# Optimization experiments

Hardware: AMD Instinct MI355X
Metric: run time of the kernel (lower is better)

## Reference

```python
import jax, jax.numpy as jnp
import numpy as np

# model dims
B_, S_, D_ = 2, 2048, 1024
D_STATE, EXPAND, HEADDIM, CHUNK, NGROUPS = 128, 2, 64, 64, 1
D_INNER = EXPAND * D_
NHEADS = D_INNER // HEADDIM  # 32 ssd heads
D_PROJ = 2 * D_INNER + 2 * NGROUPS * D_STATE + NHEADS  # 4384
H_, KV_, HD_ = 16, 4, 64  # attention heads / kv heads / head dim
ROPE_DIMS = 16
MLP_DIM = int(3.0 * D_)


def _rmsnorm(x, w=None, eps=1e-5):
    y = x * jax.lax.rsqrt(jnp.mean(x * x, axis=-1, keepdims=True) + eps)
    return y * w if w is not None else y


def _layernorm(x, w, b, eps=1e-5):
    m = jnp.mean(x, axis=-1, keepdims=True)
    v = jnp.mean((x - m) ** 2, axis=-1, keepdims=True)
    return (x - m) * jax.lax.rsqrt(v + eps) * w + b


def _segsum(x):
    # (..., T) -> (..., T, T) lower-tri cumulative sums, -inf above diag
    T = x.shape[-1]
    i = jnp.arange(T)
    xx = jnp.where(i[:, None] > i[None, :], jnp.broadcast_to(x[..., None], x.shape + (T,)), 0.0)
    s = jnp.cumsum(xx, axis=-2)
    return jnp.where(i[:, None] >= i[None, :], s, -jnp.inf)


def _ssd_chunked(x, A, B, C, chunk):
    # x:(b,s,h,p) A:(b,s,h) B,C:(b,s,g,n)
    b, s, h, p = x.shape
    g, n = B.shape[2], B.shape[3]
    if g < h:
        B = jnp.repeat(B, h // g, axis=2)
        C = jnp.repeat(C, h // g, axis=2)
    c = s // chunk
    x = x.reshape(b, c, chunk, h, p)
    A = A.reshape(b, c, chunk, h).transpose(0, 3, 1, 2)  # b h c l
    B = B.reshape(b, c, chunk, h, n)
    C = C.reshape(b, c, chunk, h, n)
    L = jnp.exp(_segsum(A))
    Y_diag = jnp.einsum('bclhn,bcshn,bhcls,bcshp->bclhp', C, B, L, x)
    A_cum = jnp.cumsum(A, axis=-1)
    decay_states = jnp.exp(A_cum[..., -1:] - A_cum)
    states = jnp.einsum('bclhn,bhcl,bclhp->bchpn', B, decay_states, x)
    decay_chunk = jnp.exp(_segsum(jnp.pad(A_cum[..., -1], ((0, 0), (0, 0), (1, 0)))))
    new_states = jnp.einsum('bhzc,bchpn->bzhpn', decay_chunk[:, :, :c, 1:c + 1], states)
    Y_off = jnp.einsum('bclhn,bchpn,bhcl->bclhp', C, new_states, jnp.exp(A_cum))
    return (Y_diag + Y_off).reshape(b, s, h, p)


def _rope_cos_sin(s, rd, base=10000.0):
    inv = 1.0 / base ** (jnp.arange(0, rd, 2, dtype=jnp.float32) / rd)
    f = jnp.outer(jnp.arange(s, dtype=jnp.float32), inv)  # (s, rd/2)
    return jnp.cos(f)[None, :, None, :], jnp.sin(f)[None, :, None, :]


def _apply_rope(x, cos, sin, rd):
    xr, xp = x[..., :rd], x[..., rd:]
    half = rd // 2
    x1, x2 = xr[..., :half], xr[..., half:]
    xr = jnp.concatenate([x1 * cos + x2 * sin, -x1 * sin + x2 * cos], axis=-1)
    return jnp.concatenate([xr, xp], axis=-1)


def _mamba_block(x, mnorm_w, in_w, out_w, Dp, dt_b, A_log, Bn_w, Cn_w):
    b, s, _ = x.shape
    h = _rmsnorm(x, mnorm_w)
    zxbcdt = h @ in_w.T
    z, xs, Bc, Cc, dt = jnp.split(
        zxbcdt,
        [D_INNER, 2 * D_INNER, 2 * D_INNER + NGROUPS * D_STATE, 2 * D_INNER + 2 * NGROUPS * D_STATE],
        axis=-1)
    dt = jax.nn.softplus(dt + dt_b)  # (b,s,nheads)
    A = -jnp.exp(A_log)  # (nheads,)
    xs = xs.reshape(b, s, NHEADS, HEADDIM)
    Bc = _rmsnorm(Bc.reshape(b, s, NGROUPS, D_STATE), Bn_w)
    Cc = _rmsnorm(Cc.reshape(b, s, NGROUPS, D_STATE), Cn_w)
    y = _ssd_chunked(xs * dt[..., None], A[None, None, :] * dt, Bc, Cc, CHUNK)
    y = y + xs * Dp[None, None, :, None]
    y = y * jax.nn.silu(z).reshape(b, s, NHEADS, HEADDIM)
    return x + y.reshape(b, s, D_INNER) @ out_w.T


def _attn_block(x, ln1_w, ln1_b, cq_w, ck_w, cv_w, cproj_w, q_gain, ln2_w, ln2_b, fc_w, proj_w):
    b, s, d = x.shape
    h = _layernorm(x, ln1_w, ln1_b)
    q = (h @ cq_w.T).reshape(b, s, H_, HD_)
    k = (h @ ck_w.T).reshape(b, s, KV_, HD_)
    v = (h @ cv_w.T).reshape(b, s, KV_, HD_)
    eps = jnp.finfo(x.dtype).eps
    q = _rmsnorm(q, eps=eps)
    k = _rmsnorm(k, eps=eps)
    cos, sin = _rope_cos_sin(s, ROPE_DIMS)
    q = _apply_rope(q, cos, sin, ROPE_DIMS)
    k = _apply_rope(k, cos, sin, ROPE_DIMS)
    q = q * q_gain[None, None, :, None]
    rep = H_ // KV_
    k = jnp.repeat(k, rep, axis=2)
    v = jnp.repeat(v, rep, axis=2)
    scores = jnp.einsum('bqhd,bkhd->bhqk', q, k) / np.float32(np.sqrt(HD_))
    i = jnp.arange(s)
    scores = jnp.where(i[:, None] >= i[None, :], scores, -jnp.inf)
    w = jax.nn.softmax(scores, axis=-1)
    y = jnp.einsum('bhqk,bkhd->bqhd', w, v).reshape(b, s, d)
    x = x + y @ cproj_w.T
    h = _layernorm(x, ln2_w, ln2_b)
    return x + jax.nn.silu(h @ fc_w.T) @ proj_w.T


def setup_inputs() -> dict:
    key = jax.random.key(0)
    ks = jax.random.split(key, 16)
    rn = lambda k, shp, sc=0.02: (jax.random.normal(k, shp, dtype=jnp.float32) * sc)
    return {
        'x': jax.random.normal(ks[0], (B_, S_, D_), dtype=jnp.float32),
        'mnorm_w': jnp.ones((D_,), jnp.float32),
        'in_proj_w': rn(ks[1], (D_PROJ, D_)),
        'out_proj_w': rn(ks[2], (D_, D_INNER)),
        'D_param': jnp.ones((NHEADS,), jnp.float32),
        'dt_bias': rn(ks[3], (NHEADS,), 0.1),
        'A_log': jnp.log(0.5 + jax.random.uniform(ks[4], (NHEADS,), dtype=jnp.float32) * 0.5),
        'Bn_w': jnp.ones((D_STATE,), jnp.float32),
        'Cn_w': jnp.ones((D_STATE,), jnp.float32),
        'ln1_w': jnp.ones((D_,), jnp.float32),
        'ln1_b': jnp.zeros((D_,), jnp.float32),
        'cq_w': rn(ks[5], (D_, D_)),
        'ck_w': rn(ks[6], (KV_ * HD_, D_)),
        'cv_w': rn(ks[7], (KV_ * HD_, D_)),
        'cproj_w': rn(ks[8], (D_, D_)),
        'q_gain': jnp.full((H_,), 5.25, jnp.float32),
        'ln2_w': jnp.ones((D_,), jnp.float32),
        'ln2_b': jnp.zeros((D_,), jnp.float32),
        'fc_w': rn(ks[9], (MLP_DIM, D_)),
        'proj_w': rn(ks[10], (D_, MLP_DIM)),
    }


def reference(x, mnorm_w, in_proj_w, out_proj_w, D_param, dt_bias, A_log, Bn_w, Cn_w,
              ln1_w, ln1_b, cq_w, ck_w, cv_w, cproj_w, q_gain, ln2_w, ln2_b, fc_w, proj_w):
    x = _mamba_block(x, mnorm_w, in_proj_w, out_proj_w, D_param, dt_bias, A_log, Bn_w, Cn_w)
    x = _attn_block(x, ln1_w, ln1_b, cq_w, ck_w, cv_w, cproj_w, q_gain, ln2_w, ln2_b, fc_w, proj_w)
    return x
```

## Files before the change

### kernel.cpp

```cpp
#include <hip/hip_runtime.h>
#include <hip/hip_bf16.h>
#include <math.h>

#define B_    2
#define S_    2048
#define D_    1024
#define DI    2048
#define NH    32
#define HD    64
#define DS    128
#define CH    64
#define NC    32
#define DP    4384
#define HATT  16
#define KVH   4
#define RD    16
#define MLP   3072
#define ROWS  (B_*S_)

typedef __bf16 bf16;
typedef __bf16 bf16x8 __attribute__((ext_vector_type(8)));
typedef __bf16 bf16x4 __attribute__((ext_vector_type(4)));
typedef float  f32x4  __attribute__((ext_vector_type(4)));

__device__ __forceinline__ void async_copy16(const void* g, void* l) {
  __builtin_amdgcn_global_load_lds(
      (const __attribute__((address_space(1))) unsigned int*)g,
      (__attribute__((address_space(3))) unsigned int*)l, 16, 0, 0);
}

__device__ __forceinline__ float waveReduceSum(float v) {
#pragma unroll
  for (int off = 32; off > 0; off >>= 1) v += __shfl_down(v, off, 64);
  return v;
}

template<int NW>
__device__ __forceinline__ float blockReduceSum(float v, float* sh) {
  v = waveReduceSum(v);
  int lane = threadIdx.x & 63, wid = threadIdx.x >> 6;
  if (lane == 0) sh[wid] = v;
  __syncthreads();
  float s = 0.f;
#pragma unroll
  for (int i = 0; i < NW; i++) s += sh[i];
  __syncthreads();
  return s;
}

struct CastSeg { const float* src; bf16* dst; int nval; int ntot; int blk0; };
struct CastArgs { CastSeg seg[8]; };

__global__ __launch_bounds__(256) void castw_all(CastArgs a) {
  int blk = blockIdx.x;
  int si = 0;
#pragma unroll
  for (int i = 1; i < 8; i++) if (blk >= a.seg[i].blk0) si = i;
  CastSeg s = a.seg[si];
  int i = ((blk - s.blk0) * 256 + threadIdx.x) * 4;
  if (i >= s.ntot) return;
  float4 v = {0.f, 0.f, 0.f, 0.f};
  if (i < s.nval) v = *(const float4*)(s.src + i);
  bf16x4 o;
  o[0] = (bf16)v.x; o[1] = (bf16)v.y; o[2] = (bf16)v.z; o[3] = (bf16)v.w;
  *(bf16x4*)(s.dst + i) = o;
}

__global__ __launch_bounds__(256) void rmsnorm_k(const float* __restrict__ x,
                                                 const float* __restrict__ w,
                                                 bf16* __restrict__ y, int n) {
  __shared__ float sh[4];
  size_t row = blockIdx.x;
  const float* xr = x + row * n;
  bf16* yr = y + row * n;
  float ss = 0.f;
  for (int i = threadIdx.x; i < n; i += 256) { float v = xr[i]; ss += v * v; }
  ss = blockReduceSum<4>(ss, sh);
  float inv = rsqrtf(ss / n + 1e-5f);
  for (int i = threadIdx.x; i < n; i += 256) yr[i] = (bf16)(xr[i] * inv * w[i]);
}

template<int ACT, typename OT>
__global__ __launch_bounds__(256) void gemm_mfma(const bf16* __restrict__ A,
                                                 const bf16* __restrict__ W,
                                                 const float* __restrict__ R,
                                                 OT* __restrict__ C,
                                                 int M, int N, int K) {
  __shared__ bf16 As[128 * 32];
  __shared__ bf16 Ws[128 * 32];
  int tid = threadIdx.x, lane = tid & 63, wave = tid >> 6;
  int mt = M >> 7;
  int bid = blockIdx.x;
  int bm = (bid % mt) * 128, bn = (bid / mt) * 128;
  const bf16* gA0 = A + (size_t)(bm + wave * 32 + (lane >> 2)) * K + (lane & 3) * 8;
  const bf16* gA1 = gA0 + (size_t)16 * K;
  const bf16* gW0 = W + (size_t)(bn + wave * 32 + (lane >> 2)) * K + (lane & 3) * 8;
  const bf16* gW1 = gW0 + (size_t)16 * K;
  bf16* lA0 = As + wave * 32 * 32;
  bf16* lA1 = lA0 + 16 * 32;
  bf16* lW0 = Ws + wave * 32 * 32;
  bf16* lW1 = lW0 + 16 * 32;
  int fr = lane & 15, fq = lane >> 4;
  int wm = wave >> 1, wn = wave & 1;
  const bf16* pA = As + (wm * 64 + fr) * 32 + fq * 8;
  const bf16* pW = Ws + (wn * 64 + fr) * 32 + fq * 8;
  f32x4 acc[4][4] = {};
  for (int k0 = 0; k0 < K; k0 += 32) {
    async_copy16(gA0, lA0);
    async_copy16(gA1, lA1);
    async_copy16(gW0, lW0);
    async_copy16(gW1, lW1);
    gA0 += 32; gA1 += 32; gW0 += 32; gW1 += 32;
    __syncthreads();
    bf16x8 af[4], bfr[4];
#pragma unroll
    for (int mi = 0; mi < 4; mi++) af[mi] = *(const bf16x8*)(pA + mi * 16 * 32);
#pragma unroll
    for (int ni = 0; ni < 4; ni++) bfr[ni] = *(const bf16x8*)(pW + ni * 16 * 32);
#pragma unroll
    for (int mi = 0; mi < 4; mi++)
#pragma unroll
      for (int ni = 0; ni < 4; ni++)
        acc[mi][ni] = __builtin_amdgcn_mfma_f32_16x16x32_bf16(af[mi], bfr[ni], acc[mi][ni], 0, 0, 0);
    __syncthreads();
  }
#pragma unroll
  for (int mi = 0; mi < 4; mi++) {
    int row = bm + wm * 64 + mi * 16 + fq * 4;
#pragma unroll
    for (int ni = 0; ni < 4; ni++) {
      int col = bn + wn * 64 + ni * 16 + fr;
      if (col < N) {
#pragma unroll
        for (int r = 0; r < 4; r++) {
          float v = acc[mi][ni][r];
          if (ACT == 1) v = v / (1.f + __expf(-v));
          if (R) v += R[(size_t)(row + r) * N + col];
          C[(size_t)(row + r) * N + col] = (OT)v;
        }
      }
    }
  }
}

__global__ __launch_bounds__(256) void gemm_sk(const bf16* __restrict__ A,
                                               const bf16* __restrict__ W,
                                               bf16* __restrict__ P,
                                               int M, int N, int K, int kchunk) {
  __shared__ bf16 As[128 * 32];
  __shared__ bf16 Ws[128 * 32];
  int tid = threadIdx.x, lane = tid & 63, wave = tid >> 6;
  int mt = M >> 7;
  int bid = blockIdx.x;
  int bm = (bid % mt) * 128, bn = (bid / mt) * 128;
  int ks = blockIdx.z;
  int kbeg = ks * kchunk;
  const bf16* gA0 = A + (size_t)(bm + wave * 32 + (lane >> 2)) * K + kbeg + (lane & 3) * 8;
  const bf16* gA1 = gA0 + (size_t)16 * K;
  const bf16* gW0 = W + (size_t)(bn + wave * 32 + (lane >> 2)) * K + kbeg + (lane & 3) * 8;
  const bf16* gW1 = gW0 + (size_t)16 * K;
  bf16* lA0 = As + wave * 32 * 32;
  bf16* lA1 = lA0 + 16 * 32;
  bf16* lW0 = Ws + wave * 32 * 32;
  bf16* lW1 = lW0 + 16 * 32;
  int fr = lane & 15, fq = lane >> 4;
  int wm = wave >> 1, wn = wave & 1;
  const bf16* pA = As + (wm * 64 + fr) * 32 + fq * 8;
  const bf16* pW = Ws + (wn * 64 + fr) * 32 + fq * 8;
  f32x4 acc[4][4] = {};
  for (int k0 = 0; k0 < kchunk; k0 += 32) {
    async_copy16(gA0, lA0);
    async_copy16(gA1, lA1);
    async_copy16(gW0, lW0);
    async_copy16(gW1, lW1);
    gA0 += 32; gA1 += 32; gW0 += 32; gW1 += 32;
    __syncthreads();
    bf16x8 af[4], bfr[4];
#pragma unroll
    for (int mi = 0; mi < 4; mi++) af[mi] = *(const bf16x8*)(pA + mi * 16 * 32);
#pragma unroll
    for (int ni = 0; ni < 4; ni++) bfr[ni] = *(const bf16x8*)(pW + ni * 16 * 32);
#pragma unroll
    for (int mi = 0; mi < 4; mi++)
#pragma unroll
      for (int ni = 0; ni < 4; ni++)
        acc[mi][ni] = __builtin_amdgcn_mfma_f32_16x16x32_bf16(af[mi], bfr[ni], acc[mi][ni], 0, 0, 0);
    __syncthreads();
  }
  bf16* Pp = P + (size_t)ks * M * N;
#pragma unroll
  for (int mi = 0; mi < 4; mi++) {
    int row = bm + wm * 64 + mi * 16 + fq * 4;
#pragma unroll
    for (int ni = 0; ni < 4; ni++) {
      int col = bn + wn * 64 + ni * 16 + fr;
#pragma unroll
      for (int r = 0; r < 4; r++)
        Pp[(size_t)(row + r) * N + col] = (bf16)acc[mi][ni][r];
    }
  }
}

__global__ __launch_bounds__(256) void reduce_ln2(const bf16* __restrict__ p0,
                                                  const bf16* __restrict__ p1,
                                                  const float* __restrict__ res,
                                                  const float* __restrict__ w,
                                                  const float* __restrict__ b,
                                                  float* __restrict__ xo,
                                                  bf16* __restrict__ ho) {
  __shared__ float sh[4];
  size_t o = (size_t)blockIdx.x * 1024;
  int i = threadIdx.x * 4;
  bf16x4 a = *(const bf16x4*)(p0 + o + i);
  bf16x4 c = *(const bf16x4*)(p1 + o + i);
  f32x4 rv = *(const f32x4*)(res + o + i);
  f32x4 v;
  float s = 0.f, s2 = 0.f;
#pragma unroll
  for (int j = 0; j < 4; j++) {
    v[j] = (float)a[j] + (float)c[j] + rv[j];
    s += v[j]; s2 += v[j] * v[j];
  }
  s  = blockReduceSum<4>(s,  sh);
  s2 = blockReduceSum<4>(s2, sh);
  float mean = s / 1024.f;
  float var  = s2 / 1024.f - mean * mean;
  float inv  = rsqrtf(var + 1e-5f);
  f32x4 wv = *(const f32x4*)(w + i);
  f32x4 bv = *(const f32x4*)(b + i);
  *(f32x4*)(xo + o + i) = v;
  bf16x4 hv;
#pragma unroll
  for (int j = 0; j < 4; j++) hv[j] = (bf16)((v[j] - mean) * inv * wv[j] + bv[j]);
  *(bf16x4*)(ho + o + i) = hv;
}

__global__ __launch_bounds__(256) void reduce_out3(const bf16* __restrict__ p0,
                                                   const bf16* __restrict__ p1,
                                                   const bf16* __restrict__ p2,
                                                   const float* __restrict__ res,
                                                   float* __restrict__ out) {
  int i = (blockIdx.x * 256 + threadIdx.x) * 4;
  bf16x4 a = *(const bf16x4*)(p0 + i);
  bf16x4 c = *(const bf16x4*)(p1 + i);
  bf16x4 d = *(const bf16x4*)(p2 + i);
  f32x4 v = *(const f32x4*)(res + i);
#pragma unroll
  for (int j = 0; j < 4; j++) v[j] += (float)a[j] + (float)c[j] + (float)d[j];
  *(f32x4*)(out + i) = v;
}

__global__ __launch_bounds__(256) void reduce_qkv(const bf16* __restrict__ P,
                                                  const float* __restrict__ q_gain,
                                                  bf16* __restrict__ q,
                                                  bf16* __restrict__ k,
                                                  bf16* __restrict__ v) {
  __shared__ float buf[1536];
  size_t row = blockIdx.x;
  size_t o = row * 1536;
  const bf16* p0 = P + o;
  const bf16* p1 = P + (size_t)ROWS * 1536 + o;
  int tid = threadIdx.x;
  for (int i = tid; i < 384; i += 256) {
    bf16x4 a = *(const bf16x4*)(p0 + i * 4);
    bf16x4 c = *(const bf16x4*)(p1 + i * 4);
    f32x4 vv;
#pragma unroll
    for (int j = 0; j < 4; j++) vv[j] = (float)a[j] + (float)c[j];
    *(f32x4*)(buf + i * 4) = vv;
  }
  __syncthreads();
  int lane = tid & 63, w = tid >> 6;
  int s = (int)(row & (S_ - 1));
  int ri = lane & 7;
  float rinv = __expf(-(float)ri * (0.125f * 9.210340371976184f));
  float ang = (float)s * rinv;
  float cs = cosf(ang), sn = sinf(ang);
#pragma unroll
  for (int j = 0; j < 6; j++) {
    int hh = w * 6 + j;
    float val = buf[hh * 64 + lane];
    if (hh < 20) {
      float ss = val * val;
#pragma unroll
      for (int off = 32; off > 0; off >>= 1) ss += __shfl_xor(ss, off, 64);
      val *= rsqrtf(ss / 64.f + 1.1920929e-7f);
      float other = __shfl_xor(val, 8, 64);
      float res = val;
      if (lane < RD) res = (lane < 8) ? (val * cs + other * sn) : (val * cs - other * sn);
      if (hh < 16) {
        res *= q_gain[hh];
        q[row * (HATT * HD) + hh * HD + lane] = (bf16)res;
      } else {
        k[row * (KVH * HD) + (hh - 16) * HD + lane] = (bf16)res;
      }
    } else {
      v[row * (KVH * HD) + (hh - 20) * HD + lane] = (bf16)val;
    }
  }
}

__global__ __launch_bounds__(256) void gemm_inproj(const bf16* __restrict__ A,
                                                   const bf16* __restrict__ W,
                                                   bf16* __restrict__ zt,
                                                   bf16* __restrict__ xt,
                                                   bf16* __restrict__ bcdt) {
  const int K = 1024;
  __shared__ bf16 As[128 * 32];
  __shared__ bf16 Ws[128 * 32];
  __shared__ bf16 Ts[64 * 136];
  int tid = threadIdx.x, lane = tid & 63, wave = tid >> 6;
  int bid = blockIdx.x;
  int bm = (bid & 31) * 128, bn = (bid >> 5) * 128;
  const bf16* gA0 = A + (size_t)(bm + wave * 32 + (lane >> 2)) * K + (lane & 3) * 8;
  const bf16* gA1 = gA0 + (size_t)16 * K;
  const bf16* gW0 = W + (size_t)(bn + wave * 32 + (lane >> 2)) * K + (lane & 3) * 8;
  const bf16* gW1 = gW0 + (size_t)16 * K;
  bf16* lA0 = As + wave * 32 * 32;
  bf16* lA1 = lA0 + 16 * 32;
  bf16* lW0 = Ws + wave * 32 * 32;
  bf16* lW1 = lW0 + 16 * 32;
  int fr = lane & 15, fq = lane >> 4;
  int wm = wave >> 1, wn = wave & 1;
  const bf16* pA = As + (wm * 64 + fr) * 32 + fq * 8;
  const bf16* pW = Ws + (wn * 64 + fr) * 32 + fq * 8;
  f32x4 acc[4][4] = {};
  for (int k0 = 0; k0 < K; k0 += 32) {
    async_copy16(gA0, lA0);
    async_copy16(gA1, lA1);
    async_copy16(gW0, lW0);
    async_copy16(gW1, lW1);
    gA0 += 32; gA1 += 32; gW0 += 32; gW1 += 32;
    __syncthreads();
    bf16x8 af[4], bfr[4];
#pragma unroll
    for (int mi = 0; mi < 4; mi++) af[mi] = *(const bf16x8*)(pA + mi * 16 * 32);
#pragma unroll
    for (int ni = 0; ni < 4; ni++) bfr[ni] = *(const bf16x8*)(pW + ni * 16 * 32);
#pragma unroll
    for (int mi = 0; mi < 4; mi++)
#pragma unroll
      for (int ni = 0; ni < 4; ni++)
        acc[mi][ni] = __builtin_amdgcn_mfma_f32_16x16x32_bf16(af[mi], bfr[ni], acc[mi][ni], 0, 0, 0);
    __syncthreads();
  }
  if (bn < 4096) {
    bf16* base = (bn < 2048) ? zt : xt;
    int bq = bm >> 11, bmS = bm & 2047;
#pragma unroll
    for (int p = 0; p < 2; p++) {
      __syncthreads();
      if (wn == p) {
#pragma unroll
        for (int mi = 0; mi < 4; mi++)
#pragma unroll
          for (int ni = 0; ni < 4; ni++) {
            bf16x4 o;
#pragma unroll
            for (int r = 0; r < 4; r++) o[r] = (bf16)acc[mi][ni][r];
            *(bf16x4*)(Ts + (ni * 16 + fr) * 136 + wm * 64 + mi * 16 + fq * 4) = o;
          }
      }
      __syncthreads();
      int hh = ((bn & 2047) + p * 64) >> 6;
      bf16* dst = base + ((size_t)(bq * NH + hh) * HD) * S_ + bmS;
#pragma unroll
      for (int i = 0; i < 4; i++) {
        int idx = tid + i * 256;
        int cl = idx >> 4, sgc = (idx & 15) * 8;
        *(bf16x8*)(dst + (size_t)cl * S_ + sgc) = *(const bf16x8*)(Ts + cl * 136 + sgc);
      }
    }
  } else {
#pragma unroll
    for (int mi = 0; mi < 4; mi++) {
      int row0m = bm + wm * 64 + mi * 16 + fq * 4;
#pragma unroll
      for (int ni = 0; ni < 4; ni++) {
        int col = bn + wn * 64 + ni * 16 + fr;
        if (col < 4384) {
#pragma unroll
          for (int r = 0; r < 4; r++)
            bcdt[(size_t)(row0m + r) * 288 + (col - 4096)] = (bf16)acc[mi][ni][r];
        }
      }
    }
  }
}

__global__ __launch_bounds__(256) void t64(const bf16* __restrict__ in, bf16* __restrict__ out,
                                           int istr, size_t io, size_t oo, int n_nt) {
  __shared__ bf16 T[64 * 72];
  int bid = blockIdx.x;
  int st = bid & 31;
  int nt = (bid >> 5) % n_nt;
  int outer = bid / (32 * n_nt);
  const bf16* ip = in + outer * io + (size_t)st * 64 * istr + nt * 64;
  int tid = threadIdx.x;
#pragma unroll
  for (int i = 0; i < 2; i++) {
    int cid = tid + i * 256; int s = cid >> 3, pc = (cid & 7) * 8;
    *(bf16x8*)(T + s * 72 + pc) = *(const bf16x8*)(ip + (size_t)s * istr + pc);
  }
  __syncthreads();
  bf16* op = out + outer * oo + (size_t)nt * 64 * 2048 + st * 64;
#pragma unroll
  for (int i = 0; i < 2; i++) {
    int cid = tid + i * 256; int p = cid >> 3, sc = (cid & 7) * 8;
    bf16x8 o;
#pragma unroll
    for (int j = 0; j < 8; j++) o[j] = T[(sc + j) * 72 + p];
    *(bf16x8*)(op + (size_t)p * 2048 + sc) = o;
  }
}

__global__ __launch_bounds__(64) void ssd_prep(const bf16* __restrict__ bcdt,
                                               const float* __restrict__ dt_bias,
                                               const float* __restrict__ A_log,
                                               float* __restrict__ dt_c,
                                               float* __restrict__ ddc,
                                               float* __restrict__ ac_c,
                                               float* __restrict__ T_out) {
  int bid = blockIdx.x;
  int c = bid % NC, hh = (bid / NC) % NH, b = bid / (NC * NH);
  int l = threadIdx.x;
  size_t row = (size_t)b * S_ + c * 64 + l;
  float raw = (float)bcdt[row * 288 + 256 + hh] + dt_bias[hh];
  float dtv = (raw > 20.f) ? raw : log1pf(__expf(raw));
  float a = -__expf(A_log[hh]) * dtv;
  float ps = a;
#pragma unroll
  for (int off = 1; off < 64; off <<= 1) {
    float t = __shfl_up(ps, off, 64);
    if (l >= off) ps += t;
  }
  float a63 = __shfl(ps, 63, 64);
  size_t o = ((size_t)b * NH + hh) * S_ + c * 64 + l;
  dt_c[o] = dtv;
  ac_c[o] = ps;
  ddc[o] = __expf(a63 - ps) * dtv;
  if (l == 63) T_out[(b * NH + hh) * NC + c] = ps;
}

__global__ __launch_bounds__(128) void bc_norm(const bf16* __restrict__ bcdt,
                                               const float* __restrict__ Bw,
                                               const float* __restrict__ Cw,
                                               bf16* __restrict__ Bn,
                                               bf16* __restrict__ Cn) {
  __shared__ float shb[2], shc[2];
  size_t row = blockIdx.x;
  int i = threadIdx.x;
  float bv = (float)bcdt[row * 288 + i];
  float cv = (float)bcdt[row * 288 + 128 + i];
  float sb = waveReduceSum(bv * bv);
  float sc = waveReduceSum(cv * cv);
  int lane = threadIdx.x & 63, wid = threadIdx.x >> 6;
  if (lane == 0) { shb[wid] = sb; shc[wid] = sc; }
  __syncthreads();
  float tb = shb[0] + shb[1];
  float tc = shc[0] + shc[1];
  Bn[row * DS + i] = (bf16)(bv * rsqrtf(tb / DS + 1e-5f) * Bw[i]);
  Cn[row * DS + i] = (bf16)(cv * rsqrtf(tc / DS + 1e-5f) * Cw[i]);
}

__global__ __launch_bounds__(256) void ssd_states(const bf16* __restrict__ Xt,
                                                  const bf16* __restrict__ Btr,
                                                  const float* __restrict__ ddc,
                                                  bf16* __restrict__ states) {
  __shared__ bf16 Xs[64 * 72];
  __shared__ bf16 Bs[128 * 72];
  int bid = blockIdx.x;
  int h = bid % NH;
  int c = (bid / NH) % NC;
  int b = bid / (NH * NC);
  int tid = threadIdx.x, lane = tid & 63, w = tid >> 6;
  int fr = lane & 15, fq = lane >> 4;
  const size_t xbase = (size_t)(b * NH + h) * HD * S_ + c * 64;
  const size_t dbase = (size_t)(b * NH + h) * S_ + c * 64;
#pragma unroll
  for (int i = 0; i < 2; i++) {
    int cid = tid + i * 256; int p = cid >> 3, sc = (cid & 7) * 8;
    bf16x8 xv = *(const bf16x8*)(Xt + xbase + (size_t)p * S_ + sc);
    f32x4 d0 = *(const f32x4*)(ddc + dbase + sc);
    f32x4 d1 = *(const f32x4*)(ddc + dbase + sc + 4);
    bf16x8 o;
#pragma unroll
    for (int j = 0; j < 4; j++) { o[j] = (bf16)((float)xv[j] * d0[j]); o[4 + j] = (bf16)((float)xv[4 + j] * d1[j]); }
    *(bf16x8*)(Xs + p * 72 + sc) = o;
  }
  const size_t bbase = (size_t)b * 128 * S_ + c * 64;
#pragma unroll
  for (int i = 0; i < 4; i++) {
    int cid = tid + i * 256; int n = cid >> 3, sc = (cid & 7) * 8;
    *(bf16x8*)(Bs + n * 72 + sc) = *(const bf16x8*)(Btr + bbase + (size_t)n * S_ + sc);
  }
  __syncthreads();
  f32x4 acc[4][2] = {};
#pragma unroll
  for (int ks = 0; ks < 2; ks++) {
    bf16x8 a[4], bb[2];
#pragma unroll
    for (int pt = 0; pt < 4; pt++) a[pt] = *(const bf16x8*)(Xs + (pt * 16 + fr) * 72 + ks * 32 + fq * 8);
#pragma unroll
    for (int n2 = 0; n2 < 2; n2++) bb[n2] = *(const bf16x8*)(Bs + ((2 * w + n2) * 16 + fr) * 72 + ks * 32 + fq * 8);
#pragma unroll
    for (int pt = 0; pt < 4; pt++)
#pragma unroll
      for (int n2 = 0; n2 < 2; n2++)
        acc[pt][n2] = __builtin_amdgcn_mfma_f32_16x16x32_bf16(a[pt], bb[n2], acc[pt][n2], 0, 0, 0);
  }
  bf16* outp = states + (size_t)bid * 8192;
#pragma unroll
  for (int pt = 0; pt < 4; pt++)
#pragma unroll
    for (int n2 = 0; n2 < 2; n2++) {
      int n = (2 * w + n2) * 16 + fr;
#pragma unroll
      for (int r = 0; r < 4; r++)
        outp[(size_t)(pt * 16 + fq * 4 + r) * 128 + n] = (bf16)acc[pt][n2][r];
    }
}

__global__ __launch_bounds__(256) void ssd_scan(bf16* __restrict__ states,
                                                const float* __restrict__ T) {
  __shared__ float eT[NC];
  int part = blockIdx.x & 7;
  int bh = blockIdx.x >> 3;
  int b = bh / NH, h = bh % NH;
  if (threadIdx.x < NC) eT[threadIdx.x] = __expf(T[(size_t)(b * NH + h) * NC + threadIdx.x]);
  __syncthreads();
  const size_t cstride = (size_t)NH * HD * DS;
  size_t base = ((size_t)b * NC * NH + h) * (HD * DS);
#pragma unroll
  for (int j = 0; j < 4; j++) {
    int e = part * 1024 + threadIdx.x + j * 256;
    float carry = 0.f;
    size_t idx = base + e;
    for (int c = 0; c < NC; c++) {
      float sv = (float)states[idx];
      states[idx] = (bf16)carry;
      carry = sv + eT[c] * carry;
      idx += cstride;
    }
  }
}

__global__ __launch_bounds__(256) void ssd_out(const bf16* __restrict__ Cn,
                                               const bf16* __restrict__ Bn,
                                               const bf16* __restrict__ Xt,
                                               const bf16* __restrict__ Zt,
                                               const float* __restrict__ dt_c,
                                               const float* __restrict__ ac_c,
                                               const bf16* __restrict__ states,
                                               const float* __restrict__ Dp,
                                               bf16* __restrict__ ybf) {
  __shared__ bf16 Cs[64 * 136];
  __shared__ bf16 BNs[64 * 136];
  __shared__ bf16 Xs[64 * 72];
  __shared__ bf16 G[64 * 72];
  __shared__ float acs[64];
  int bid = blockIdx.x;
  int h = bid % NH;
  int c = (bid / NH) % NC;
  int b = bid / (NH * NC);
  int tid = threadIdx.x, lane = tid & 63, w = tid >> 6;
  int fr = lane & 15, fq = lane >> 4;
  size_t row0 = (size_t)b * S_ + c * 64;
  const size_t abase = (size_t)(b * NH + h) * S_ + c * 64;
  if (tid < 64) acs[tid] = ac_c[abase + tid];
#pragma unroll
  for (int i = 0; i < 4; i++) {
    int cid = tid + i * 256; int l = cid >> 4, nc = (cid & 15) * 8;
    float e = __expf(ac_c[abase + l]);
    bf16x8 cv = *(const bf16x8*)(Cn + (row0 + l) * DS + nc);
    bf16x8 o;
#pragma unroll
    for (int j = 0; j < 8; j++) o[j] = (bf16)((float)cv[j] * e);
    *(bf16x8*)(Cs + l * 136 + nc) = o;
    *(bf16x8*)(BNs + l * 136 + nc) = *(const bf16x8*)(Bn + (row0 + l) * DS + nc);
  }
  const size_t xbase = (size_t)(b * NH + h) * HD * S_ + c * 64;
#pragma unroll
  for (int i = 0; i < 2; i++) {
    int cid = tid + i * 256; int p = cid >> 3, sc = (cid & 7) * 8;
    bf16x8 xv = *(const bf16x8*)(Xt + xbase + (size_t)p * S_ + sc);
    f32x4 d0 = *(const f32x4*)(dt_c + abase + sc);
    f32x4 d1 = *(const f32x4*)(dt_c + abase + sc + 4);
    bf16x8 o;
#pragma unroll
    for (int j = 0; j < 4; j++) { o[j] = (bf16)((float)xv[j] * d0[j]); o[4 + j] = (bf16)((float)xv[4 + j] * d1[j]); }
    *(bf16x8*)(Xs + p * 72 + sc) = o;
  }
  __syncthreads();
  bf16x8 ca[4];
#pragma unroll
  for (int ks = 0; ks < 4; ks++) ca[ks] = *(const bf16x8*)(Cs + (w * 16 + fr) * 136 + ks * 32 + fq * 8);
  f32x4 cb[4] = {};
  for (int st = 0; st <= w; st++)
#pragma unroll
    for (int ks = 0; ks < 4; ks++)
      cb[st] = __builtin_amdgcn_mfma_f32_16x16x32_bf16(ca[ks],
                 *(const bf16x8*)(BNs + (st * 16 + fr) * 136 + ks * 32 + fq * 8), cb[st], 0, 0, 0);
#pragma unroll
  for (int st = 0; st < 4; st++) {
    float es = (st <= w) ? __expf(-acs[st * 16 + fr]) : 0.f;
#pragma unroll
    for (int r = 0; r < 4; r++) {
      int lloc = fq * 4 + r;
      float g = 0.f;
      if (st < w) g = cb[st][r] * es;
      else if (st == w) g = (lloc >= fr) ? cb[st][r] * es : 0.f;
      G[(w * 16 + lloc) * 72 + st * 16 + fr] = (bf16)g;
    }
  }
  f32x4 acc[4] = {};
  {
    bf16x8 ga0 = *(const bf16x8*)(G + (w * 16 + fr) * 72 + fq * 8);
    bf16x8 ga1 = *(const bf16x8*)(G + (w * 16 + fr) * 72 + 32 + fq * 8);
#pragma unroll
    for (int pt = 0; pt < 4; pt++) {
      acc[pt] = __builtin_amdgcn_mfma_f32_16x16x32_bf16(ga0,
                  *(const bf16x8*)(Xs + (pt * 16 + fr) * 72 + fq * 8), acc[pt], 0, 0, 0);
      acc[pt] = __builtin_amdgcn_mfma_f32_16x16x32_bf16(ga1,
                  *(const bf16x8*)(Xs + (pt * 16 + fr) * 72 + 32 + fq * 8), acc[pt], 0, 0, 0);
    }
  }
  __syncthreads();
  const bf16* stp = states + (size_t)bid * 8192;
#pragma unroll
  for (int i = 0; i < 4; i++) {
    int cid = tid + i * 256; int p = cid >> 4, nc = (cid & 15) * 8;
    *(bf16x8*)(BNs + p * 136 + nc) = *(const bf16x8*)(stp + (size_t)p * 128 + nc);
  }
  __syncthreads();
#pragma unroll
  for (int pt = 0; pt < 4; pt++)
#pragma unroll
    for (int ks = 0; ks < 4; ks++)
      acc[pt] = __builtin_amdgcn_mfma_f32_16x16x32_bf16(ca[ks],
                  *(const bf16x8*)(BNs + (pt * 16 + fr) * 136 + ks * 32 + fq * 8), acc[pt], 0, 0, 0);
  float dph = Dp[h];
#pragma unroll
  for (int pt = 0; pt < 4; pt++) {
    int p = pt * 16 + fr;
    size_t tb = (xbase + (size_t)p * S_) + w * 16 + fq * 4;
    bf16x4 xs4 = *(const bf16x4*)(Xt + tb);
    bf16x4 z4  = *(const bf16x4*)(Zt + tb);
#pragma unroll
    for (int r = 0; r < 4; r++) {
      int l = w * 16 + fq * 4 + r;
      float yv = acc[pt][r] + (float)xs4[r] * dph;
      float z = (float)z4[r];
      yv *= z / (1.f + __expf(-z));
      ybf[((row0 + l) * NH + h) * HD + p] = (bf16)yv;
    }
  }
}

#define KSTR 72
#define PSTR 72
__global__ __launch_bounds__(256) void attn_mfma(const bf16* __restrict__ q,
                                                 const bf16* __restrict__ k,
                                                 const bf16* __restrict__ vtr,
                                                 bf16* __restrict__ Po,
                                                 float* __restrict__ Ls) {
  __shared__ bf16 Ks[64 * KSTR];
  __shared__ bf16 Vs[64 * KSTR];
  __shared__ bf16 Pl[4][32 * PSTR];
  int c = 39 - blockIdx.x;
  int g = (c < 4) ? 0 : (c < 12) ? 1 : (c < 24) ? 2 : 3;
  int gbase = (g == 0) ? 0 : (g == 1) ? 4 : (g == 2) ? 12 : 24;
  int d = c - gbase;
  int qt = 4 * g + d / (g + 1);
  int sk = d % (g + 1);
  int h = blockIdx.y, b = blockIdx.z;
  int kvh = h >> 2;
  int tid = threadIdx.x, lane = tid & 63, w = tid >> 6;
  int fr = lane & 15, fq = lane >> 4;
  const float SC = 0.18033688011112042f;
  const float M2 = 62.0f;
  int kt0 = sk * 8;
  int ktend = min(kt0 + 8, 2 * qt + 2);
  int qbase = qt * 128 + w * 32;
  int qmaxw = qbase + 31;
  bf16x8 bq[2][2];
#pragma unroll
  for (int qc = 0; qc < 2; qc++)
#pragma unroll
    for (int ks = 0; ks < 2; ks++)
      bq[qc][ks] = *(const bf16x8*)(q + (size_t)(b * S_ + qbase + qc * 16 + fr) * (HATT * HD)
                                      + h * HD + ks * 32 + fq * 8);
  int sr = tid >> 3, sc8 = (tid & 7) * 8;
  const bf16* kg = k + ((size_t)(b * S_) + sr) * (KVH * HD) + kvh * HD + sc8;
  const bf16* vg = vtr + ((size_t)(b * KVH + kvh) * HD + sr) * S_ + sc8;
  bf16x8 krg0, krg1, vrg0, vrg1;
  {
    const bf16* kp = kg + (size_t)kt0 * 64 * (KVH * HD);
    const bf16* vp = vg + (size_t)kt0 * 64;
    krg0 = *(const bf16x8*)(kp);
    krg1 = *(const bf16x8*)(kp + (size_t)32 * (KVH * HD));
    vrg0 = *(const bf16x8*)(vp);
    vrg1 = *(const bf16x8*)(vp + (size_t)32 * S_);
  }
  float lsum[2] = {0.f, 0.f};
  f32x4 yacc[2][4] = {};
  bf16* Plw = Pl[w];
  for (int kt = kt0; kt < ktend; kt++) {
    __syncthreads();
    *(bf16x8*)(&Ks[sr * KSTR + sc8]) = krg0;
    *(bf16x8*)(&Ks[(sr + 32) * KSTR + sc8]) = krg1;
    *(bf16x8*)(&Vs[sr * KSTR + sc8]) = vrg0;
    *(bf16x8*)(&Vs[(sr + 32) * KSTR + sc8]) = vrg1;
    __syncthreads();
    if ((kt + 1) < ktend) {
      const bf16* kp = kg + (size_t)(kt + 1) * 64 * (KVH * HD);
      const bf16* vp = vg + (size_t)(kt + 1) * 64;
      krg0 = *(const bf16x8*)(kp);
      krg1 = *(const bf16x8*)(kp + (size_t)32 * (KVH * HD));
      vrg0 = *(const bf16x8*)(vp);
      vrg1 = *(const bf16x8*)(vp + (size_t)32 * S_);
    }
    if (kt * 64 <= qmaxw) {
      bool nomask = (kt * 64 + 63) <= qbase;
      if (nomask) {
#pragma unroll
        for (int mi = 0; mi < 4; mi++) {
          const bf16* krow = &Ks[(mi * 16 + fr) * KSTR];
          bf16x8 ak0 = *(const bf16x8*)(krow + fq * 8);
          bf16x8 ak1 = *(const bf16x8*)(krow + 32 + fq * 8);
#pragma unroll
          for (int qc = 0; qc < 2; qc++) {
            f32x4 s = {};
            s = __builtin_amdgcn_mfma_f32_16x16x32_bf16(ak0, bq[qc][0], s, 0, 0, 0);
            s = __builtin_amdgcn_mfma_f32_16x16x32_bf16(ak1, bq[qc][1], s, 0, 0, 0);
            bf16x4 pk;
#pragma unroll
            for (int r = 0; r < 4; r++) {
              float p = __builtin_amdgcn_exp2f(s[r] * SC - M2);
              lsum[qc] += p;
              pk[r] = (bf16)p;
            }
            *(bf16x4*)(Plw + (qc * 16 + fr) * PSTR + mi * 16 + fq * 4) = pk;
          }
        }
      } else {
#pragma unroll
        for (int mi = 0; mi < 4; mi++) {
          int s0 = kt * 64 + mi * 16;
          if (s0 > qmaxw) {
            bf16x4 zz = {};
#pragma unroll
            for (int qc = 0; qc < 2; qc++)
              *(bf16x4*)(Plw + (qc * 16 + fr) * PSTR + mi * 16 + fq * 4) = zz;
          } else {
            const bf16* krow = &Ks[(mi * 16 + fr) * KSTR];
            bf16x8 ak0 = *(const bf16x8*)(krow + fq * 8);
            bf16x8 ak1 = *(const bf16x8*)(krow + 32 + fq * 8);
#pragma unroll
            for (int qc = 0; qc < 2; qc++) {
              f32x4 s = {};
              s = __builtin_amdgcn_mfma_f32_16x16x32_bf16(ak0, bq[qc][0], s, 0, 0, 0);
              s = __builtin_amdgcn_mfma_f32_16x16x32_bf16(ak1, bq[qc][1], s, 0, 0, 0);
              int qq = qbase + qc * 16 + fr;
              bf16x4 pk;
#pragma unroll
              for (int r = 0; r < 4; r++) {
                int sp = s0 + fq * 4 + r;
                float p = (sp <= qq) ? __builtin_amdgcn_exp2f(s[r] * SC - M2) : 0.f;
                lsum[qc] += p;
                pk[r] = (bf16)p;
              }
              *(bf16x4*)(Plw + (qc * 16 + fr) * PSTR + mi * 16 + fq * 4) = pk;
            }
          }
        }
      }
#pragma unroll
      for (int ks2 = 0; ks2 < 2; ks2++) {
        bf16x8 bp[2];
#pragma unroll
        for (int qc = 0; qc < 2; qc++)
          bp[qc] = *(const bf16x8*)(Plw + (qc * 16 + fr) * PSTR + ks2 * 32 + fq * 8);
#pragma unroll
        for (int pi = 0; pi < 4; pi++) {
          bf16x8 av = *(const bf16x8*)(&Vs[(pi * 16 + fr) * KSTR + ks2 * 32 + fq * 8]);
#pragma unroll
          for (int qc = 0; qc < 2; qc++)
            yacc[qc][pi] = __builtin_amdgcn_mfma_f32_16x16x32_bf16(av, bp[qc], yacc[qc][pi], 0, 0, 0);
        }
      }
    }
  }
#pragma unroll
  for (int qc = 0; qc < 2; qc++) {
    lsum[qc] += __shfl_xor(lsum[qc], 16, 64);
    lsum[qc] += __shfl_xor(lsum[qc], 32, 64);
    int qrow = qt * 128 + w * 32 + qc * 16 + fr;
    if (fq == 0)
      Ls[((size_t)(b * 16 + h) * 2048 + qrow) * 4 + sk] = lsum[qc];
    bf16* pop = Po + ((((size_t)(b * 16 + h) * 16 + qt) * 4 + sk) * 128
                       + w * 32 + qc * 16 + fr) * 64 + fq * 4;
#pragma unroll
    for (int pi = 0; pi < 4; pi++) {
      bf16x4 o;
#pragma unroll
      for (int r = 0; r < 4; r++) o[r] = (bf16)yacc[qc][pi][r];
      *(bf16x4*)(pop + pi * 16) = o;
    }
  }
}

__global__ __launch_bounds__(256) void attn_red(const bf16* __restrict__ Po,
                                                const float* __restrict__ Ls,
                                                bf16* __restrict__ y2) {
  int row = blockIdx.x;
  int b = row >> 11;
  int qrow = row & 2047;
  int qt = qrow >> 7, r = qrow & 127;
  int nch = (qt >> 2) + 1;
  int t = threadIdx.x;
  int h = t >> 4, e4 = (t & 15) << 2;
  const float* lp = Ls + ((size_t)(b * 16 + h) * 2048 + qrow) * 4;
  float ls = 0.f;
  f32x4 acc = {};
  for (int sk = 0; sk < nch; sk++) {
    ls += lp[sk];
    const bf16* pp = Po + ((((size_t)(b * 16 + h) * 16 + qt) * 4 + sk) * 128 + r) * 64 + e4;
    bf16x4 v = *(const bf16x4*)(pp);
#pragma unroll
    for (int j = 0; j < 4; j++) acc[j] += (float)v[j];
  }
  float inv = 1.f / ls;
  bf16x4 o;
#pragma unroll
  for (int j = 0; j < 4; j++) o[j] = (bf16)(acc[j] * inv);
  *(bf16x4*)(y2 + (size_t)row * 1024 + h * 64 + e4) = o;
}

constexpr size_t OFF_WIN  = 0;
constexpr size_t OFF_WOUT = 9175040;
constexpr size_t OFF_WQKV = 13369344;
constexpr size_t OFF_WCP  = 16515072;
constexpr size_t OFF_WFC  = 18612224;
constexpr size_t OFF_WPR  = 24903680;
constexpr size_t OFF_HBF  = 31195136;
constexpr size_t OFF_BCDT = 39583744;
constexpr size_t OFF_XT   = 41943040;
constexpr size_t OFF_ZT   = 58720256;
constexpr size_t OFF_DTC  = 75497472;
constexpr size_t OFF_DDC  = 76546048;
constexpr size_t OFF_ACC  = 77594624;
constexpr size_t OFF_T    = 78643200;
constexpr size_t OFF_BN   = 78651392;
constexpr size_t OFF_CN   = 79699968;
constexpr size_t OFF_BTR  = 80748544;
constexpr size_t OFF_ST   = 81797120;
constexpr size_t OFF_YBF  = 148905984;
constexpr size_t OFF_X1   = 165683200;
constexpr size_t OFF_P    = OFF_ST;
constexpr size_t OFF_PO   = OFF_ST;
constexpr size_t OFF_LS   = OFF_BCDT;
constexpr size_t OFF_QB   = OFF_XT;
constexpr size_t OFF_KB   = OFF_XT + 8388608;
constexpr size_t OFF_VB   = OFF_XT + 10485760;
constexpr size_t OFF_VTR  = OFF_XT + 12582912;
constexpr size_t OFF_Y2   = OFF_ZT;
constexpr size_t OFF_X2   = 50331648;
constexpr size_t OFF_MLP  = 132128768;

extern "C" void kernel_launch(void* const* d_in, const int* in_sizes, int n_in,
                              void* d_out, int out_size, void* d_ws, size_t ws_size,
                              hipStream_t stream) {
  (void)in_sizes; (void)n_in; (void)out_size; (void)ws_size;
  const float* x        = (const float*)d_in[0];
  const float* mnorm_w  = (const float*)d_in[1];
  const float* in_w     = (const float*)d_in[2];
  const float* out_w    = (const float*)d_in[3];
  const float* Dp       = (const float*)d_in[4];
  const float* dt_bias  = (const float*)d_in[5];
  const float* A_log    = (const float*)d_in[6];
  const float* Bn_w     = (const float*)d_in[7];
  const float* Cn_w     = (const float*)d_in[8];
  const float* ln1_w    = (const float*)d_in[9];
  const float* ln1_b    = (const float*)d_in[10];
  const float* cq_w     = (const float*)d_in[11];
  const float* ck_w     = (const float*)d_in[12];
  const float* cv_w     = (const float*)d_in[13];
  const float* cproj_w  = (const float*)d_in[14];
  const float* q_gain   = (const float*)d_in[15];
  const float* ln2_w    = (const float*)d_in[16];
  const float* ln2_b    = (const float*)d_in[17];
  const float* fc_w     = (const float*)d_in[18];
  const float* proj_w   = (const float*)d_in[19];
  float* out = (float*)d_out;
  char* W8 = (char*)d_ws;

  bf16* w_in   = (bf16*)(W8 + OFF_WIN);
  bf16* w_out  = (bf16*)(W8 + OFF_WOUT);
  bf16* w_qkv  = (bf16*)(W8 + OFF_WQKV);
  bf16* w_cp   = (bf16*)(W8 + OFF_WCP);
  bf16* w_fc   = (bf16*)(W8 + OFF_WFC);
  bf16* w_pr   = (bf16*)(W8 + OFF_WPR);
  bf16* h_bf   = (bf16*)(W8 + OFF_HBF);
  bf16* bcdt   = (bf16*)(W8 + OFF_BCDT);
  bf16* Xt     = (bf16*)(W8 + OFF_XT);
  bf16* Zt     = (bf16*)(W8 + OFF_ZT);
  float* dt_c  = (float*)(W8 + OFF_DTC);
  float* ddc   = (float*)(W8 + OFF_DDC);
  float* ac_c  = (float*)(W8 + OFF_ACC);
  float* Tb    = (float*)(W8 + OFF_T);
  bf16* Bn     = (bf16*)(W8 + OFF_BN);
  bf16* Cn     = (bf16*)(W8 + OFF_CN);
  bf16* Btr    = (bf16*)(W8 + OFF_BTR);
  bf16* st     = (bf16*)(W8 + OFF_ST);
  bf16* ybf    = (bf16*)(W8 + OFF_YBF);
  float* x1    = (float*)(W8 + OFF_X1);
  bf16* Pbuf   = (bf16*)(W8 + OFF_P);
  bf16* Po     = (bf16*)(W8 + OFF_PO);
  float* Ls    = (float*)(W8 + OFF_LS);
  bf16* qbf    = (bf16*)(W8 + OFF_QB);
  bf16* kbf    = (bf16*)(W8 + OFF_KB);
  bf16* vbf    = (bf16*)(W8 + OFF_VB);
  bf16* vtr    = (bf16*)(W8 + OFF_VTR);
  bf16* y2     = (bf16*)(W8 + OFF_Y2);
  float* x2    = (float*)(W8 + OFF_X2);
  bf16* mlp    = (bf16*)(W8 + OFF_MLP);

  CastArgs ca;
  ca.seg[0] = { in_w,    w_in,            4489216, 4587520, 0     };
  ca.seg[1] = { out_w,   w_out,           2097152, 2097152, 4480  };
  ca.seg[2] = { cq_w,    w_qkv,           1048576, 1048576, 6528  };
  ca.seg[3] = { ck_w,    w_qkv + 1048576,  262144,  262144, 7552  };
  ca.seg[4] = { cv_w,    w_qkv + 1310720,  262144,  262144, 7808  };
  ca.seg[5] = { cproj_w, w_cp,            1048576, 1048576, 8064  };
  ca.seg[6] = { fc_w,    w_fc,            3145728, 3145728, 9088  };
  ca.seg[7] = { proj_w,  w_pr,            3145728, 3145728, 12160 };
  castw_all<<<15232, 256, 0, stream>>>(ca);

  const size_t PS  = (size_t)ROWS * 1024;

  rmsnorm_k<<<ROWS, 256, 0, stream>>>(x, mnorm_w, h_bf, D_);
  gemm_inproj<<<32 * 35, 256, 0, stream>>>(h_bf, w_in, Zt, Xt, bcdt);
  ssd_prep<<<B_ * NH * NC, 64, 0, stream>>>(bcdt, dt_bias, A_log, dt_c, ddc, ac_c, Tb);
  bc_norm<<<ROWS, 128, 0, stream>>>(bcdt, Bn_w, Cn_w, Bn, Cn);
  t64<<<2 * 2 * 32, 256, 0, stream>>>(Bn, Btr, 128, (size_t)2048 * 128, (size_t)128 * 2048, 2);
  ssd_states<<<B_ * NC * NH, 256, 0, stream>>>(Xt, Btr, ddc, st);
  ssd_scan<<<B_ * NH * 8, 256, 0, stream>>>(st, Tb);
  ssd_out<<<B_ * NC * NH, 256, 0, stream>>>(Cn, Bn, Xt, Zt, dt_c, ac_c, st, Dp, ybf);
  gemm_sk<<<dim3(32 * 8, 1, 2), 256, 0, stream>>>(ybf, w_out, Pbuf, ROWS, D_, DI, 1024);
  reduce_ln2<<<ROWS, 256, 0, stream>>>(Pbuf, Pbuf + PS, x, ln1_w, ln1_b, x1, h_bf);

  gemm_sk<<<dim3(32 * 12, 1, 2), 256, 0, stream>>>(h_bf, w_qkv, Pbuf, ROWS, 1536, D_, 512);
  reduce_qkv<<<ROWS, 256, 0, stream>>>(Pbuf, q_gain, qbf, kbf, vbf);
  t64<<<2 * 4 * 32, 256, 0, stream>>>(vbf, vtr, 256, (size_t)2048 * 256, (size_t)256 * 2048, 4);
  attn_mfma<<<dim3(40, HATT, B_), 256, 0, stream>>>(qbf, kbf, vtr, Po, Ls);
  attn_red<<<ROWS, 256, 0, stream>>>(Po, Ls, y2);
  gemm_sk<<<dim3(32 * 8, 1, 2), 256, 0, stream>>>(y2, w_cp, Pbuf, ROWS, D_, D_, 512);
  reduce_ln2<<<ROWS, 256, 0, stream>>>(Pbuf, Pbuf + PS, x1, ln2_w, ln2_b, x2, h_bf);

  gemm_mfma<1, bf16><<<32 * 24, 256, 0, stream>>>(h_bf, w_fc, nullptr, mlp, ROWS, MLP, D_);
  gemm_sk<<<dim3(32 * 8, 1, 3), 256, 0, stream>>>(mlp, w_pr, Pbuf, ROWS, D_, MLP, 1024);
  reduce_out3<<<ROWS, 256, 0, stream>>>(Pbuf, Pbuf + PS, Pbuf + 2 * PS, x2, out);
}
```

Baseline: 515.2 us.

## Rewrite in-projection GEMM with 256x256 tiles, triple-buffered async loads, LDS swizzle

The in-projection GEMM moves from 128x128 tiles on 256 threads to 256x256 tiles on 512 threads. It adds a three-stage async-copy pipeline with explicit vmcnt waits and a single barrier per K step, an XOR swizzle on LDS rows to avoid bank conflicts, s_setprio around the MFMA block, and a remapped block order for L2 locality. The goal is more data reuse per tile and hiding global-load latency behind compute. In exchange it uses more registers and LDS, and launches only 288 blocks (256 of them on the 4096 zt/xt columns), so the whole grid fits in one wave of CUs but leaves no spare blocks to balance load.

```diff
diff --git a/kernel.cpp b/kernel.cpp
--- a/kernel.cpp
+++ b/kernel.cpp
@@ -300,88 +300,110 @@
   }
 }
 
-__global__ __launch_bounds__(256) void gemm_inproj(const bf16* __restrict__ A,
-                                                   const bf16* __restrict__ W,
-                                                   bf16* __restrict__ zt,
-                                                   bf16* __restrict__ xt,
-                                                   bf16* __restrict__ bcdt) {
-  const int K = 1024;
-  __shared__ bf16 As[128 * 32];
-  __shared__ bf16 Ws[128 * 32];
-  __shared__ bf16 Ts[64 * 136];
-  int tid = threadIdx.x, lane = tid & 63, wave = tid >> 6;
+__global__ __launch_bounds__(512, 2) void gemm256_inproj(const bf16* __restrict__ A,
+                                                         const bf16* __restrict__ W,
+                                                         bf16* __restrict__ zt,
+                                                         bf16* __restrict__ xt,
+                                                         bf16* __restrict__ bcdt) {
+  __shared__ bf16 lds[3 * 16384];
+  int tid = threadIdx.x;
+  int lane = tid & 63, w = tid >> 6;
+  int wm = w >> 2, wn = w & 3;
+  int fr = lane & 15, fq = lane >> 4;
   int bid = blockIdx.x;
-  int bm = (bid & 31) * 128, bn = (bid >> 5) * 128;
-  const bf16* gA0 = A + (size_t)(bm + wave * 32 + (lane >> 2)) * K + (lane & 3) * 8;
-  const bf16* gA1 = gA0 + (size_t)16 * K;
-  const bf16* gW0 = W + (size_t)(bn + wave * 32 + (lane >> 2)) * K + (lane & 3) * 8;
-  const bf16* gW1 = gW0 + (size_t)16 * K;
-  bf16* lA0 = As + wave * 32 * 32;
-  bf16* lA1 = lA0 + 16 * 32;
-  bf16* lW0 = Ws + wave * 32 * 32;
-  bf16* lW1 = lW0 + 16 * 32;
-  int fr = lane & 15, fq = lane >> 4;
-  int wm = wave >> 1, wn = wave & 1;
-  const bf16* pA = As + (wm * 64 + fr) * 32 + fq * 8;
-  const bf16* pW = Ws + (wn * 64 + fr) * 32 + fq * 8;
-  f32x4 acc[4][4] = {};
-  for (int k0 = 0; k0 < K; k0 += 32) {
-    async_copy16(gA0, lA0);
-    async_copy16(gA1, lA1);
-    async_copy16(gW0, lW0);
-    async_copy16(gW1, lW1);
-    gA0 += 32; gA1 += 32; gW0 += 32; gW1 += 32;
-    __syncthreads();
-    bf16x8 af[4], bfr[4];
-#pragma unroll
-    for (int mi = 0; mi < 4; mi++) af[mi] = *(const bf16x8*)(pA + mi * 16 * 32);
-#pragma unroll
-    for (int ni = 0; ni < 4; ni++) bfr[ni] = *(const bf16x8*)(pW + ni * 16 * 32);
-#pragma unroll
-    for (int mi = 0; mi < 4; mi++)
+  bid = (bid & 7) * 36 + (bid >> 3);
+  int bm = (bid & 15) * 256;
+  int bn = (bid >> 4) * 256;
+  int srow = w * 32 + (lane >> 2);
+  int sswz = (lane & 3) ^ ((lane >> 2) & 3);
+  const bf16* gA = A + (size_t)(bm + srow) * 1024 + sswz * 8;
+  const bf16* gW = W + (size_t)(bn + srow) * 1024 + sswz * 8;
+  int sbase = w * 32 * 32;
+  int rdswz = (fq ^ (fr & 3)) * 8;
+  f32x4 acc[8][4] = {};
+  {
+    bf16* bA = lds + sbase;
+    bf16* bB = lds + 8192 + sbase;
+    async_copy16(gA, bA);
+    async_copy16(gA + 16 * 1024, bA + 16 * 32);
+    async_copy16(gW, bB);
+    async_copy16(gW + 16 * 1024, bB + 16 * 32);
+  }
+  int cur = 0, nxt = 1;
+  for (int t = 0; t < 32; t++) {
+    if (t + 1 < 32) {
+      const bf16* ga = gA + (t + 1) * 32;
+      const bf16* gw = gW + (t + 1) * 32;
+      bf16* bA = lds + nxt * 16384 + sbase;
+      bf16* bB = lds + nxt * 16384 + 8192 + sbase;
+      async_copy16(ga, bA);
+      async_copy16(ga + 16 * 1024, bA + 16 * 32);
+      async_copy16(gw, bB);
+      async_copy16(gw + 16 * 1024, bB + 16 * 32);
+      asm volatile("s_waitcnt vmcnt(4)" ::: "memory");
+    } else {
+      asm volatile("s_waitcnt vmcnt(0)" ::: "memory");
+    }
+    __builtin_amdgcn_sched_barrier(0);
+    __builtin_amdgcn_s_barrier();
+    __builtin_amdgcn_sched_barrier(0);
+    const bf16* cA = lds + cur * 16384;
+    const bf16* cB = cA + 8192;
+    bf16x8 af[8], bfv[4];
+#pragma unroll
+    for (int mi = 0; mi < 8; mi++)
+      af[mi] = *(const bf16x8*)(cA + (wm * 128 + mi * 16 + fr) * 32 + rdswz);
+#pragma unroll
+    for (int ni = 0; ni < 4; ni++)
+      bfv[ni] = *(const bf16x8*)(cB + (wn * 64 + ni * 16 + fr) * 32 + rdswz);
+    __builtin_amdgcn_s_setprio(1);
+#pragma unroll
+    for (int mi = 0; mi < 8; mi++)
 #pragma unroll
       for (int ni = 0; ni < 4; ni++)
-        acc[mi][ni] = __builtin_amdgcn_mfma_f32_16x16x32_bf16(af[mi], bfr[ni], acc[mi][ni], 0, 0, 0);
-    __syncthreads();
+        acc[mi][ni] = __builtin_amdgcn_mfma_f32_16x16x32_bf16(af[mi], bfv[ni], acc[mi][ni], 0, 0, 0);
+    __builtin_amdgcn_s_setprio(0);
+    cur = nxt; nxt = nxt + 1; if (nxt == 3) nxt = 0;
   }
   if (bn < 4096) {
     bf16* base = (bn < 2048) ? zt : xt;
     int bq = bm >> 11, bmS = bm & 2047;
-#pragma unroll
-    for (int p = 0; p < 2; p++) {
+    bf16* Ts = lds;
+#pragma unroll 1
+    for (int g = 0; g < 4; g++) {
       __syncthreads();
-      if (wn == p) {
-#pragma unroll
-        for (int mi = 0; mi < 4; mi++)
+      if (wn == g) {
+#pragma unroll
+        for (int mi = 0; mi < 8; mi++)
 #pragma unroll
           for (int ni = 0; ni < 4; ni++) {
             bf16x4 o;
 #pragma unroll
             for (int r = 0; r < 4; r++) o[r] = (bf16)acc[mi][ni][r];
-            *(bf16x4*)(Ts + (ni * 16 + fr) * 136 + wm * 64 + mi * 16 + fq * 4) = o;
+            *(bf16x4*)(Ts + (ni * 16 + fr) * 264 + wm * 128 + mi * 16 + fq * 4) = o;
           }
       }
       __syncthreads();
-      int hh = ((bn & 2047) + p * 64) >> 6;
+      int hh = ((bn & 2047) + g * 64) >> 6;
       bf16* dst = base + ((size_t)(bq * NH + hh) * HD) * S_ + bmS;
 #pragma unroll
       for (int i = 0; i < 4; i++) {
-        int idx = tid + i * 256;
-        int cl = idx >> 4, sgc = (idx & 15) * 8;
-        *(bf16x8*)(dst + (size_t)cl * S_ + sgc) = *(const bf16x8*)(Ts + cl * 136 + sgc);
+        int idx = tid + i * 512;
+        int p = idx >> 5, sc = (idx & 31) * 8;
+        *(bf16x8*)(dst + (size_t)p * S_ + sc) = *(const bf16x8*)(Ts + p * 264 + sc);
       }
     }
   } else {
 #pragma unroll
-    for (int mi = 0; mi < 4; mi++) {
-      int row0m = bm + wm * 64 + mi * 16 + fq * 4;
+    for (int mi = 0; mi < 8; mi++) {
+      int row = bm + wm * 128 + mi * 16 + fq * 4;
 #pragma unroll
       for (int ni = 0; ni < 4; ni++) {
         int col = bn + wn * 64 + ni * 16 + fr;
         if (col < 4384) {
 #pragma unroll
           for (int r = 0; r < 4; r++)
-            bcdt[(size_t)(row0m + r) * 288 + (col - 4096)] = (bf16)acc[mi][ni][r];
+            bcdt[(size_t)(row + r) * 288 + (col - 4096)] = (bf16)acc[mi][ni][r];
         }
       }
     }
@@ -940,7 +962,7 @@
   const size_t PS  = (size_t)ROWS * 1024;
 
   rmsnorm_k<<<ROWS, 256, 0, stream>>>(x, mnorm_w, h_bf, D_);
-  gemm_inproj<<<32 * 35, 256, 0, stream>>>(h_bf, w_in, Zt, Xt, bcdt);
+  gemm256_inproj<<<288, 512, 0, stream>>>(h_bf, w_in, Zt, Xt, bcdt);
   ssd_prep<<<B_ * NH * NC, 64, 0, stream>>>(bcdt, dt_bias, A_log, dt_c, ddc, ac_c, Tb);
   bc_norm<<<ROWS, 128, 0, stream>>>(bcdt, Bn_w, Cn_w, Bn, Cn);
   t64<<<2 * 2 * 32, 256, 0, stream>>>(Bn, Btr, 128, (size_t)2048 * 128, (size_t)128 * 2048, 2);
```

Measured after the change: 530.5 us. 3.0% more time.
